# Optimization experiments

Measured on AMD Instinct MI355X. Metric: run time of the kernel, lower is better.

The kernel has to match this reference:

```python
import jax, jax.numpy as jnp
import numpy as np

L = 16          # trellis state bits -> expanded LUT size 2**16
TLUT_BITS = 10  # base codebook bits -> tlut has 2**10 entries
ENC_SHAPE = (16384, 2048)


def quantlut_sym_2d(tlut, Lbits, nbits):
    # Faithful port of quantlut_sym_2d: bitwise hash + 2-channel sign flip.
    idx = jnp.arange(1 << Lbits, dtype=jnp.uint32)
    h = (idx + jnp.uint32(1)) * idx            # max 65536*65535 < 2**32, no overflow
    sflp0 = 1.0 - ((h >> 15) & 1).astype(tlut.dtype) * 2.0
    sflp1 = 1.0 - ((h >> 13) & 1).astype(tlut.dtype) * 2.0
    sel = ((h >> (16 - nbits - 1)) & ((1 << nbits) - 1)).astype(jnp.int32)
    # [2**L, 2] = base codebook gather * per-channel sign flips
    return tlut[sel] * jnp.stack([sflp0, sflp1], axis=-1)


def setup_inputs() -> dict:
    key = jax.random.key(0)
    k1, k2 = jax.random.split(key)
    tlut = jax.random.normal(k1, (1 << TLUT_BITS, 2), dtype=jnp.float32)
    encoded = jax.random.randint(k2, ENC_SHAPE, 0, 1 << L, dtype=jnp.int32)
    return {"tlut": tlut, "encoded": encoded}


def reference(tlut, encoded):
    # recons(): dequantize trellis codes via expanded sign-flipped LUT gather.
    lut = quantlut_sym_2d(tlut, L, TLUT_BITS)   # [65536, 2]
    return lut[encoded]                          # [16384, 2048, 2]
```

## Files before the change

kernel.cpp:

```cpp
#include <hip/hip_runtime.h>
#include <hip/hip_bf16.h>
#include <stdint.h>


constexpr int TLUT_ENTRIES = 1024;
constexpr int BLOCK = 256;

typedef float f32x4 __attribute__((ext_vector_type(4)));

__global__ __launch_bounds__(BLOCK) void trellis_dequant_kernel(
    const float2*   __restrict__ tlut,
    const uint64_t* __restrict__ enc,
    f32x4*          __restrict__ out,
    int n2)
{
    __shared__ float2 slut[TLUT_ENTRIES];
    for (int j = threadIdx.x; j < TLUT_ENTRIES; j += BLOCK)
        slut[j] = tlut[j];
    __syncthreads();

    const int stride = gridDim.x * BLOCK;
    int i = blockIdx.x * BLOCK + threadIdx.x;
    #pragma unroll 2
    for (; i < n2; i += stride) {
        uint64_t e2 = __builtin_nontemporal_load(&enc[i]);
        uint32_t e0 = (uint32_t)e2;
        uint32_t e1 = (uint32_t)(e2 >> 32);
        uint32_t h0 = (e0 + 1u) * e0;
        uint32_t h1 = (e1 + 1u) * e1;

        float2 t0 = slut[(h0 >> 5) & 1023u];
        float2 t1 = slut[(h1 >> 5) & 1023u];

        uint32_t s00 = (h0 & 0x8000u) << 16;
        uint32_t s01 = (h0 & 0x2000u) << 18;
        uint32_t s10 = (h1 & 0x8000u) << 16;
        uint32_t s11 = (h1 & 0x2000u) << 18;

        f32x4 o;
        o.x = __uint_as_float(__float_as_uint(t0.x) ^ s00);
        o.y = __uint_as_float(__float_as_uint(t0.y) ^ s01);
        o.z = __uint_as_float(__float_as_uint(t1.x) ^ s10);
        o.w = __uint_as_float(__float_as_uint(t1.y) ^ s11);
        __builtin_nontemporal_store(o, &out[i]);
    }
}

extern "C" void kernel_launch(void* const* d_in, const int* in_sizes, int n_in,
                              void* d_out, int out_size, void* d_ws, size_t ws_size,
                              hipStream_t stream) {
    const float2*   tlut = (const float2*)d_in[0];
    const uint64_t* enc  = (const uint64_t*)d_in[1];
    f32x4*          out  = (f32x4*)d_out;

    const int n_codes = in_sizes[1];
    const int n2 = n_codes / 2;

    const int blocks = 8192;
    trellis_dequant_kernel<<<blocks, BLOCK, 0, stream>>>(tlut, enc, out, n2);
}
```

Baseline: 358.3 us.

## Process four codes per thread with 16B loads and split SoA LDS table

Each thread now loads four codes with one 16-byte nontemporal load and writes two 16-byte output vectors, where it previously handled two codes with an 8-byte load. The shared codebook is split into separate x and y arrays, and the grid drops from 8192 to 2048 blocks. The aim is fewer, wider memory transactions and less loop overhead. In exchange each output store now has a 32-byte stride per thread, which may reduce store coalescing, and the smaller grid may leave less parallelism for hiding memory latency.

New measurement: 381.0 us. +6.3%, slower.

```diff
diff --git a/kernel.cpp b/kernel.cpp
--- a/kernel.cpp
+++ b/kernel.cpp
@@ -1,61 +1,74 @@
 #include <hip/hip_runtime.h>
-#include <hip/hip_bf16.h>
 #include <stdint.h>
 
 
 constexpr int TLUT_ENTRIES = 1024;
 constexpr int BLOCK = 256;
+constexpr int GRID  = 2048;
 
-typedef float f32x4 __attribute__((ext_vector_type(4)));
+typedef float    f32x4 __attribute__((ext_vector_type(4)));
+typedef uint32_t u32x4 __attribute__((ext_vector_type(4)));
 
 __global__ __launch_bounds__(BLOCK) void trellis_dequant_kernel(
-    const float2*   __restrict__ tlut,
-    const uint64_t* __restrict__ enc,
-    f32x4*          __restrict__ out,
-    int n2)
+    const float2* __restrict__ tlut,
+    const u32x4*  __restrict__ enc,
+    f32x4*        __restrict__ out,
+    int n4)
 {
-    __shared__ float2 slut[TLUT_ENTRIES];
-    for (int j = threadIdx.x; j < TLUT_ENTRIES; j += BLOCK)
-        slut[j] = tlut[j];
+    __shared__ float sx[TLUT_ENTRIES];
+    __shared__ float sy[TLUT_ENTRIES];
+    for (int j = threadIdx.x; j < TLUT_ENTRIES; j += BLOCK) {
+        float2 t = tlut[j];
+        sx[j] = t.x;
+        sy[j] = t.y;
+    }
     __syncthreads();
 
-    const int stride = gridDim.x * BLOCK;
+    const int stride = GRID * BLOCK;
     int i = blockIdx.x * BLOCK + threadIdx.x;
     #pragma unroll 2
-    for (; i < n2; i += stride) {
-        uint64_t e2 = __builtin_nontemporal_load(&enc[i]);
-        uint32_t e0 = (uint32_t)e2;
-        uint32_t e1 = (uint32_t)(e2 >> 32);
-        uint32_t h0 = (e0 + 1u) * e0;
-        uint32_t h1 = (e1 + 1u) * e1;
+    for (; i < n4; i += stride) {
+        u32x4 e4 = __builtin_nontemporal_load(&enc[i]);
 
-        float2 t0 = slut[(h0 >> 5) & 1023u];
-        float2 t1 = slut[(h1 >> 5) & 1023u];
+        uint32_t h0 = (e4.x + 1u) * e4.x;
+        uint32_t h1 = (e4.y + 1u) * e4.y;
+        uint32_t h2 = (e4.z + 1u) * e4.z;
+        uint32_t h3 = (e4.w + 1u) * e4.w;
 
-        uint32_t s00 = (h0 & 0x8000u) << 16;
-        uint32_t s01 = (h0 & 0x2000u) << 18;
-        uint32_t s10 = (h1 & 0x8000u) << 16;
-        uint32_t s11 = (h1 & 0x2000u) << 18;
+        uint32_t i0 = (h0 >> 5) & 1023u;
+        uint32_t i1 = (h1 >> 5) & 1023u;
+        uint32_t i2 = (h2 >> 5) & 1023u;
+        uint32_t i3 = (h3 >> 5) & 1023u;
 
-        f32x4 o;
-        o.x = __uint_as_float(__float_as_uint(t0.x) ^ s00);
-        o.y = __uint_as_float(__float_as_uint(t0.y) ^ s01);
-        o.z = __uint_as_float(__float_as_uint(t1.x) ^ s10);
-        o.w = __uint_as_float(__float_as_uint(t1.y) ^ s11);
-        __builtin_nontemporal_store(o, &out[i]);
+        float x0 = sx[i0], y0 = sy[i0];
+        float x1 = sx[i1], y1 = sy[i1];
+        float x2 = sx[i2], y2 = sy[i2];
+        float x3 = sx[i3], y3 = sy[i3];
+
+        f32x4 oA, oB;
+        oA.x = __uint_as_float(__float_as_uint(x0) ^ ((h0 & 0x8000u) << 16));
+        oA.y = __uint_as_float(__float_as_uint(y0) ^ ((h0 & 0x2000u) << 18));
+        oA.z = __uint_as_float(__float_as_uint(x1) ^ ((h1 & 0x8000u) << 16));
+        oA.w = __uint_as_float(__float_as_uint(y1) ^ ((h1 & 0x2000u) << 18));
+        oB.x = __uint_as_float(__float_as_uint(x2) ^ ((h2 & 0x8000u) << 16));
+        oB.y = __uint_as_float(__float_as_uint(y2) ^ ((h2 & 0x2000u) << 18));
+        oB.z = __uint_as_float(__float_as_uint(x3) ^ ((h3 & 0x8000u) << 16));
+        oB.w = __uint_as_float(__float_as_uint(y3) ^ ((h3 & 0x2000u) << 18));
+
+        __builtin_nontemporal_store(oA, &out[2 * i]);
+        __builtin_nontemporal_store(oB, &out[2 * i + 1]);
     }
 }
 
 extern "C" void kernel_launch(void* const* d_in, const int* in_sizes, int n_in,
                               void* d_out, int out_size, void* d_ws, size_t ws_size,
                               hipStream_t stream) {
-    const float2*   tlut = (const float2*)d_in[0];
-    const uint64_t* enc  = (const uint64_t*)d_in[1];
-    f32x4*          out  = (f32x4*)d_out;
+    const float2* tlut = (const float2*)d_in[0];
+    const u32x4*  enc  = (const u32x4*)d_in[1];
+    f32x4*        out  = (f32x4*)d_out;
 
     const int n_codes = in_sizes[1];
-    const int n2 = n_codes / 2;
+    const int n4 = n_codes / 4;
 
-    const int blocks = 8192;
-    trellis_dequant_kernel<<<blocks, BLOCK, 0, stream>>>(tlut, enc, out, n2);
+    trellis_dequant_kernel<<<GRID, BLOCK, 0, stream>>>(tlut, enc, out, n4);
 }
```
